# Performance work log

Hardware: AMD Instinct MI355X
Metric: run time of the kernel (lower is better)

## Reference

```python
import jax, jax.numpy as jnp
import numpy as np

B, S, H, NH = 8, 1024, 768, 12
DK = H // NH  # 64


def setup_inputs() -> dict:
    key = jax.random.key(0)
    ks = jax.random.split(key, 7)
    sc = 0.02
    return {
        "Q": jax.random.normal(ks[0], (B, S, H), jnp.float32),
        "K": jax.random.normal(ks[1], (B, S, H), jnp.float32),
        "V": jax.random.normal(ks[2], (B, S, H), jnp.float32),
        "Wq": jax.random.normal(ks[3], (H, H), jnp.float32) * sc,
        "Wk": jax.random.normal(ks[4], (H, H), jnp.float32) * sc,
        "Wv": jax.random.normal(ks[5], (H, H), jnp.float32) * sc,
        "Wo": jax.random.normal(ks[6], (H, H), jnp.float32) * sc,
    }


def reference(Q, K, V, Wq, Wk, Wv, Wo):
    # torch Linear(bias=False): y = x @ W.T, weight shape [out, in]
    q = jnp.einsum('bsh,oh->bso', Q, Wq).reshape(B, S, NH, DK)
    k = jnp.einsum('bsh,oh->bso', K, Wk).reshape(B, S, NH, DK)
    v = jnp.einsum('bsh,oh->bso', V, Wv).reshape(B, S, NH, DK)
    # naive SDPA per head: full [B,NH,S,S] score matrix, scale by sqrt(dk)
    scores = jnp.einsum('bqnd,bknd->bnqk', q, k) / jnp.sqrt(jnp.float32(DK))
    w = jax.nn.softmax(scores, axis=-1)
    c = jnp.einsum('bnqk,bknd->bqnd', w, v).reshape(B, S, H)
    return jnp.einsum('bsh,oh->bso', c, Wo)
```

## Files before the change

### kernel.cpp

```cpp
#include <hip/hip_runtime.h>
#include <hip/hip_bf16.h>

#define B_   8
#define S_   1024
#define H_   768
#define NH_  12
#define DK_  64
#define M_   (B_ * S_)

typedef __attribute__((ext_vector_type(8))) short          short8;
typedef __attribute__((ext_vector_type(8))) unsigned short ushort8;
typedef __attribute__((ext_vector_type(4))) unsigned short ushort4v;
typedef __attribute__((ext_vector_type(4))) float          f32x4;

__device__ __forceinline__ unsigned short f2bf(float x) {
    union { __hip_bfloat16 h; unsigned short u; } r;
    r.h = __float2bfloat16(x);
    return r.u;
}

__global__ __launch_bounds__(256)
void cvt_w(const float* __restrict__ w0, const float* __restrict__ w1,
           const float* __restrict__ w2, const float* __restrict__ w3,
           unsigned short* __restrict__ o0, unsigned short* __restrict__ o1,
           unsigned short* __restrict__ o2, unsigned short* __restrict__ o3)
{
    const int wsel = blockIdx.y;
    const float* src = (wsel == 0) ? w0 : (wsel == 1) ? w1 : (wsel == 2) ? w2 : w3;
    unsigned short* dst = (wsel == 0) ? o0 : (wsel == 1) ? o1 : (wsel == 2) ? o2 : o3;
    const float s = (wsel == 0) ? 0.125f * 1.44269504089f : 1.0f;
    const int i = blockIdx.x * 256 + threadIdx.x;
    const float4 x = ((const float4*)src)[i];
    ushort4v o;
    o[0] = f2bf(x.x * s); o[1] = f2bf(x.y * s);
    o[2] = f2bf(x.z * s); o[3] = f2bf(x.w * s);
    ((ushort4v*)dst)[i] = o;
}

template<bool A_BF16, bool OUT_BF16>
__global__ __launch_bounds__(256)
void gemm_bt(const void* __restrict__ A0, const void* __restrict__ A1,
             const void* __restrict__ A2,
             const unsigned short* __restrict__ W0,
             const unsigned short* __restrict__ W1,
             const unsigned short* __restrict__ W2,
             void* __restrict__ C0, void* __restrict__ C1, void* __restrict__ C2)
{
    __shared__ unsigned short As[128 * 32];
    __shared__ unsigned short Bs[128 * 32];

    const int tid  = threadIdx.x;
    const int z    = blockIdx.z;
    const int bm   = blockIdx.x, bn = blockIdx.y;
    const int w    = tid >> 6, lane = tid & 63;
    const int lg   = lane >> 4, lc = lane & 15;
    const int wm   = (w >> 1) * 64, wn = (w & 1) * 64;

    const void* Av = (z == 0) ? A0 : (z == 1) ? A1 : A2;
    const unsigned short* Bw = (z == 0) ? W0 : (z == 1) ? W1 : W2;
    void* Cv = (z == 0) ? C0 : (z == 1) ? C1 : C2;

    const float*          Af = (const float*)Av;
    const unsigned short* Ah = (const unsigned short*)Av;

    f32x4 acc[4][4] = {};

    for (int k0 = 0; k0 < H_; k0 += 32) {
        if (A_BF16) {
#pragma unroll
            for (int i = 0; i < 2; i++) {
                const int gI = i * 256 + tid;
                const int row = gI >> 2, c8 = (gI & 3) * 8;
                *(ushort8*)&As[row * 32 + c8] =
                    *(const ushort8*)&Ah[(size_t)(bm * 128 + row) * H_ + k0 + c8];
            }
        } else {
#pragma unroll
            for (int i = 0; i < 4; i++) {
                const int gI = i * 256 + tid;
                const int row = gI >> 3, c4 = (gI & 7) * 4;
                const float4 x = *(const float4*)&Af[(size_t)(bm * 128 + row) * H_ + k0 + c4];
                ushort4v o4;
                o4[0] = f2bf(x.x); o4[1] = f2bf(x.y);
                o4[2] = f2bf(x.z); o4[3] = f2bf(x.w);
                *(ushort4v*)&As[row * 32 + c4] = o4;
            }
        }
#pragma unroll
        for (int i = 0; i < 2; i++) {
            const int gI = i * 256 + tid;
            const int row = gI >> 2, c8 = (gI & 3) * 8;
            *(ushort8*)&Bs[row * 32 + c8] =
                *(const ushort8*)&Bw[(size_t)(bn * 128 + row) * H_ + k0 + c8];
        }
        __syncthreads();

        short8 af[4], bfr[4];
#pragma unroll
        for (int mi = 0; mi < 4; mi++)
            af[mi] = *(const short8*)&As[(wm + mi * 16 + lc) * 32 + lg * 8];
#pragma unroll
        for (int ni = 0; ni < 4; ni++)
            bfr[ni] = *(const short8*)&Bs[(wn + ni * 16 + lc) * 32 + lg * 8];
#pragma unroll
        for (int mi = 0; mi < 4; mi++)
#pragma unroll
            for (int ni = 0; ni < 4; ni++)
                acc[mi][ni] = __builtin_amdgcn_mfma_f32_16x16x32_bf16(
                    af[mi], bfr[ni], acc[mi][ni], 0, 0, 0);
        __syncthreads();
    }

#pragma unroll
    for (int mi = 0; mi < 4; mi++)
#pragma unroll
        for (int ni = 0; ni < 4; ni++)
#pragma unroll
            for (int reg = 0; reg < 4; reg++) {
                const int row = bm * 128 + wm + mi * 16 + lg * 4 + reg;
                const int col = bn * 128 + wn + ni * 16 + lc;
                if (OUT_BF16)
                    ((unsigned short*)Cv)[(size_t)row * H_ + col] = f2bf(acc[mi][ni][reg]);
                else
                    ((float*)Cv)[(size_t)row * H_ + col] = acc[mi][ni][reg];
            }
}

__global__ __launch_bounds__(256)
void attn(const unsigned short* __restrict__ q,
          const unsigned short* __restrict__ k,
          const unsigned short* __restrict__ v,
          unsigned short* __restrict__ c)
{
    __shared__ unsigned short Ks[64][72];
    __shared__ unsigned short Vt[64][72];
    __shared__ unsigned short Ps[128][72];

    const int tid  = threadIdx.x;
    const int qt   = blockIdx.x, h = blockIdx.y, b = blockIdx.z;
    const int wid  = tid >> 6;
    const int lane = tid & 63;
    const int lg   = lane >> 4, lc = lane & 15;
    const int r    = tid >> 2;
    const int d0   = (tid & 3) * 16;
    const int g    = tid & 3;
    const size_t base = (size_t)b * S_ * H_ + (size_t)h * DK_;

#pragma unroll
    for (int rr = 0; rr < 128; rr += 64) {
        const unsigned short* src = &q[base + (size_t)(qt * 128 + rr + r) * H_ + d0];
        *(ushort8*)&Ps[rr + r][d0]     = *(const ushort8*)src;
        *(ushort8*)&Ps[rr + r][d0 + 8] = *(const ushort8*)(src + 8);
    }
    __syncthreads();
    short8 aq[2][2];
#pragma unroll
    for (int m = 0; m < 2; m++)
#pragma unroll
        for (int ks = 0; ks < 2; ks++)
            aq[m][ks] = *(const short8*)&Ps[wid * 32 + m * 16 + lc][ks * 32 + lg * 8];

    f32x4 o[2][4] = {};
    float mrow[2][4], lrow[2][4];
#pragma unroll
    for (int m = 0; m < 2; m++)
#pragma unroll
        for (int i = 0; i < 4; i++) { mrow[m][i] = -1e30f; lrow[m][i] = 0.f; }

    for (int kt = 0; kt < S_ / 64; kt++) {
        {
            const unsigned short* ksrc = &k[base + (size_t)(kt * 64 + r) * H_ + d0];
            *(ushort8*)&Ks[r][d0]     = *(const ushort8*)ksrc;
            *(ushort8*)&Ks[r][d0 + 8] = *(const ushort8*)(ksrc + 8);
            const unsigned short* vsrc = &v[base + (size_t)(kt * 64 + r) * H_ + d0];
            const ushort8 v0 = *(const ushort8*)vsrc;
            const ushort8 v1 = *(const ushort8*)(vsrc + 8);
            const int colv = r ^ (g << 4);
#pragma unroll
            for (int j = 0; j < 8; j++) Vt[d0 + j][colv]     = v0[j];
#pragma unroll
            for (int j = 0; j < 8; j++) Vt[d0 + 8 + j][colv] = v1[j];
        }
        __syncthreads();

        f32x4 s[2][4] = {};
#pragma unroll
        for (int ni = 0; ni < 4; ni++) {
            const short8 bk0 = *(const short8*)&Ks[ni * 16 + lc][lg * 8];
            const short8 bk1 = *(const short8*)&Ks[ni * 16 + lc][32 + lg * 8];
            s[0][ni] = __builtin_amdgcn_mfma_f32_16x16x32_bf16(aq[0][0], bk0, s[0][ni], 0, 0, 0);
            s[0][ni] = __builtin_amdgcn_mfma_f32_16x16x32_bf16(aq[0][1], bk1, s[0][ni], 0, 0, 0);
            s[1][ni] = __builtin_amdgcn_mfma_f32_16x16x32_bf16(aq[1][0], bk0, s[1][ni], 0, 0, 0);
            s[1][ni] = __builtin_amdgcn_mfma_f32_16x16x32_bf16(aq[1][1], bk1, s[1][ni], 0, 0, 0);
        }

#pragma unroll
        for (int m = 0; m < 2; m++)
#pragma unroll
            for (int reg = 0; reg < 4; reg++) {
                float pm = fmaxf(fmaxf(s[m][0][reg], s[m][1][reg]),
                                 fmaxf(s[m][2][reg], s[m][3][reg]));
#pragma unroll
                for (int d = 1; d < 16; d <<= 1)
                    pm = fmaxf(pm, __shfl_xor(pm, d, 64));
                const float mnew  = fmaxf(mrow[m][reg], pm);
                const float scale = exp2f(mrow[m][reg] - mnew);
                float psum = 0.f;
#pragma unroll
                for (int ni = 0; ni < 4; ni++) {
                    const float p = exp2f(s[m][ni][reg] - mnew);
                    s[m][ni][reg] = p; psum += p;
                }
#pragma unroll
                for (int d = 1; d < 16; d <<= 1)
                    psum += __shfl_xor(psum, d, 64);
                lrow[m][reg] = lrow[m][reg] * scale + psum;
                mrow[m][reg] = mnew;
                o[m][0][reg] *= scale; o[m][1][reg] *= scale;
                o[m][2][reg] *= scale; o[m][3][reg] *= scale;
            }

#pragma unroll
        for (int m = 0; m < 2; m++)
#pragma unroll
            for (int ni = 0; ni < 4; ni++)
#pragma unroll
                for (int reg = 0; reg < 4; reg++)
                    Ps[wid * 32 + m * 16 + lg * 4 + reg][(ni * 16 + lc) ^ (lg << 4)] =
                        f2bf(s[m][ni][reg]);

        short8 pa[2][2];
#pragma unroll
        for (int m = 0; m < 2; m++)
#pragma unroll
            for (int ks = 0; ks < 2; ks++)
                pa[m][ks] = *(const short8*)
                    &Ps[wid * 32 + m * 16 + lc][(ks * 32 + lg * 8) ^ ((lc >> 2) << 4)];
#pragma unroll
        for (int ni = 0; ni < 4; ni++)
#pragma unroll
            for (int ks = 0; ks < 2; ks++) {
                const short8 bv = *(const short8*)
                    &Vt[ni * 16 + lc][(ks * 32 + lg * 8) ^ (ni << 4)];
                o[0][ni] = __builtin_amdgcn_mfma_f32_16x16x32_bf16(pa[0][ks], bv, o[0][ni], 0, 0, 0);
                o[1][ni] = __builtin_amdgcn_mfma_f32_16x16x32_bf16(pa[1][ks], bv, o[1][ni], 0, 0, 0);
            }
        __syncthreads();
    }

#pragma unroll
    for (int m = 0; m < 2; m++)
#pragma unroll
        for (int reg = 0; reg < 4; reg++) {
            const float inv = 1.0f / lrow[m][reg];
            const int row = qt * 128 + wid * 32 + m * 16 + lg * 4 + reg;
#pragma unroll
            for (int ni = 0; ni < 4; ni++)
                c[base + (size_t)row * H_ + ni * 16 + lc] = f2bf(o[m][ni][reg] * inv);
        }
}

extern "C" void kernel_launch(void* const* d_in, const int* in_sizes, int n_in,
                              void* d_out, int out_size, void* d_ws, size_t ws_size,
                              hipStream_t stream)
{
    const float* Q  = (const float*)d_in[0];
    const float* K  = (const float*)d_in[1];
    const float* V  = (const float*)d_in[2];
    const float* Wq = (const float*)d_in[3];
    const float* Wk = (const float*)d_in[4];
    const float* Wv = (const float*)d_in[5];
    const float* Wo = (const float*)d_in[6];

    unsigned short* qb = (unsigned short*)d_ws;
    unsigned short* kb = qb + (size_t)M_ * H_;
    unsigned short* vb = kb + (size_t)M_ * H_;
    unsigned short* cb = vb + (size_t)M_ * H_;
    unsigned short* wq = cb + (size_t)M_ * H_;
    unsigned short* wk = wq + (size_t)H_ * H_;
    unsigned short* wv = wk + (size_t)H_ * H_;
    unsigned short* wo = wv + (size_t)H_ * H_;

    cvt_w<<<dim3(H_ * H_ / 4 / 256, 4), 256, 0, stream>>>(
        Wq, Wk, Wv, Wo, wq, wk, wv, wo);

    gemm_bt<false, true><<<dim3(M_ / 128, H_ / 128, 3), 256, 0, stream>>>(
        Q, K, V, wq, wk, wv, qb, kb, vb);

    attn<<<dim3(S_ / 128, NH_, B_), 256, 0, stream>>>(qb, kb, vb, cb);

    gemm_bt<true, false><<<dim3(M_ / 128, H_ / 128, 1), 256, 0, stream>>>(
        cb, cb, cb, wo, wo, wo, d_out, d_out, d_out);
}
```

Baseline: 180.8 us.

## Compute transposed scores in attention and pass P via shuffles instead of LDS

The QK^T MFMA now has its operands swapped, so each lane holds the scores for a single query row. The row max and sum then need only two cross-lane shuffles instead of four per register. The probability tile is packed to bf16 with v_cvt_pk_bf16_f32 and rearranged into the PV A-operand layout with register shuffles, which removes the Ps shared buffer, its stores and loads, and a sync. Q fragments are read straight from global memory, and the per-row scale is broadcast by shuffle. This trades LDS traffic for more cross-lane shuffle and select instructions.

```diff
diff --git a/kernel.cpp b/kernel.cpp
--- a/kernel.cpp
+++ b/kernel.cpp
@@ -17,6 +17,12 @@
     union { __hip_bfloat16 h; unsigned short u; } r;
     r.h = __float2bfloat16(x);
     return r.u;
+}
+
+__device__ __forceinline__ unsigned cvtpk_bf16(float lo, float hi) {
+    unsigned r;
+    asm("v_cvt_pk_bf16_f32 %0, %1, %2" : "=v"(r) : "v"(lo), "v"(hi));
+    return r;
 }
 
 __global__ __launch_bounds__(256)
@@ -134,7 +140,6 @@
 {
     __shared__ unsigned short Ks[64][72];
     __shared__ unsigned short Vt[64][72];
-    __shared__ unsigned short Ps[128][72];
 
     const int tid  = threadIdx.x;
     const int qt   = blockIdx.x, h = blockIdx.y, b = blockIdx.z;
@@ -146,26 +151,16 @@
     const int g    = tid & 3;
     const size_t base = (size_t)b * S_ * H_ + (size_t)h * DK_;
 
-#pragma unroll
-    for (int rr = 0; rr < 128; rr += 64) {
-        const unsigned short* src = &q[base + (size_t)(qt * 128 + rr + r) * H_ + d0];
-        *(ushort8*)&Ps[rr + r][d0]     = *(const ushort8*)src;
-        *(ushort8*)&Ps[rr + r][d0 + 8] = *(const ushort8*)(src + 8);
-    }
-    __syncthreads();
     short8 aq[2][2];
 #pragma unroll
     for (int m = 0; m < 2; m++)
 #pragma unroll
         for (int ks = 0; ks < 2; ks++)
-            aq[m][ks] = *(const short8*)&Ps[wid * 32 + m * 16 + lc][ks * 32 + lg * 8];
+            aq[m][ks] = *(const short8*)
+                &q[base + (size_t)(qt * 128 + wid * 32 + m * 16 + lc) * H_ + ks * 32 + lg * 8];
 
     f32x4 o[2][4] = {};
-    float mrow[2][4], lrow[2][4];
-#pragma unroll
-    for (int m = 0; m < 2; m++)
-#pragma unroll
-        for (int i = 0; i < 4; i++) { mrow[m][i] = -1e30f; lrow[m][i] = 0.f; }
+    float mrow[2] = {-1e30f, -1e30f}, lrow[2] = {0.f, 0.f};
 
     for (int kt = 0; kt < S_ / 64; kt++) {
         {
@@ -183,59 +178,81 @@
         }
         __syncthreads();
 
-        f32x4 s[2][4] = {};
-#pragma unroll
-        for (int ni = 0; ni < 4; ni++) {
-            const short8 bk0 = *(const short8*)&Ks[ni * 16 + lc][lg * 8];
-            const short8 bk1 = *(const short8*)&Ks[ni * 16 + lc][32 + lg * 8];
-            s[0][ni] = __builtin_amdgcn_mfma_f32_16x16x32_bf16(aq[0][0], bk0, s[0][ni], 0, 0, 0);
-            s[0][ni] = __builtin_amdgcn_mfma_f32_16x16x32_bf16(aq[0][1], bk1, s[0][ni], 0, 0, 0);
-            s[1][ni] = __builtin_amdgcn_mfma_f32_16x16x32_bf16(aq[1][0], bk0, s[1][ni], 0, 0, 0);
-            s[1][ni] = __builtin_amdgcn_mfma_f32_16x16x32_bf16(aq[1][1], bk1, s[1][ni], 0, 0, 0);
-        }
-
+        f32x4 st[2][4] = {};
+#pragma unroll
+        for (int ni = 0; ni < 4; ni++)
+#pragma unroll
+            for (int ks = 0; ks < 2; ks++) {
+                const short8 bk = *(const short8*)&Ks[ni * 16 + lc][ks * 32 + lg * 8];
+                st[0][ni] = __builtin_amdgcn_mfma_f32_16x16x32_bf16(bk, aq[0][ks], st[0][ni], 0, 0, 0);
+                st[1][ni] = __builtin_amdgcn_mfma_f32_16x16x32_bf16(bk, aq[1][ks], st[1][ni], 0, 0, 0);
+            }
+
+        unsigned pw[2][4][2];
+#pragma unroll
+        for (int m = 0; m < 2; m++) {
+            float pm = st[m][0][0];
+#pragma unroll
+            for (int ni = 0; ni < 4; ni++)
+#pragma unroll
+                for (int reg = 0; reg < 4; reg++)
+                    pm = fmaxf(pm, st[m][ni][reg]);
+            pm = fmaxf(pm, __shfl_xor(pm, 16, 64));
+            pm = fmaxf(pm, __shfl_xor(pm, 32, 64));
+            const float mnew  = fmaxf(mrow[m], pm);
+            const float scale = exp2f(mrow[m] - mnew);
+            float psum = 0.f;
+#pragma unroll
+            for (int ni = 0; ni < 4; ni++)
+#pragma unroll
+                for (int reg = 0; reg < 4; reg++) {
+                    const float p = exp2f(st[m][ni][reg] - mnew);
+                    st[m][ni][reg] = p; psum += p;
+                }
+            psum += __shfl_xor(psum, 16, 64);
+            psum += __shfl_xor(psum, 32, 64);
+            lrow[m] = lrow[m] * scale + psum;
+            mrow[m] = mnew;
+
+            float scr[4];
+#pragma unroll
+            for (int reg = 0; reg < 4; reg++)
+                scr[reg] = __shfl(scale, lg * 4 + reg, 64);
+#pragma unroll
+            for (int ni = 0; ni < 4; ni++)
+#pragma unroll
+                for (int reg = 0; reg < 4; reg++)
+                    o[m][ni][reg] *= scr[reg];
+
+#pragma unroll
+            for (int ni = 0; ni < 4; ni++) {
+                pw[m][ni][0] = cvtpk_bf16(st[m][ni][0], st[m][ni][1]);
+                pw[m][ni][1] = cvtpk_bf16(st[m][ni][2], st[m][ni][3]);
+            }
+        }
+
+        const int sl0 = lc + ((lg & 1) << 5);
+        const int sl1 = sl0 + 16;
+        const bool hi = (lg >> 1) != 0;
+        short8 pa[2][2];
 #pragma unroll
         for (int m = 0; m < 2; m++)
 #pragma unroll
-            for (int reg = 0; reg < 4; reg++) {
-                float pm = fmaxf(fmaxf(s[m][0][reg], s[m][1][reg]),
-                                 fmaxf(s[m][2][reg], s[m][3][reg]));
-#pragma unroll
-                for (int d = 1; d < 16; d <<= 1)
-                    pm = fmaxf(pm, __shfl_xor(pm, d, 64));
-                const float mnew  = fmaxf(mrow[m][reg], pm);
-                const float scale = exp2f(mrow[m][reg] - mnew);
-                float psum = 0.f;
-#pragma unroll
-                for (int ni = 0; ni < 4; ni++) {
-                    const float p = exp2f(s[m][ni][reg] - mnew);
-                    s[m][ni][reg] = p; psum += p;
-                }
-#pragma unroll
-                for (int d = 1; d < 16; d <<= 1)
-                    psum += __shfl_xor(psum, d, 64);
-                lrow[m][reg] = lrow[m][reg] * scale + psum;
-                mrow[m][reg] = mnew;
-                o[m][0][reg] *= scale; o[m][1][reg] *= scale;
-                o[m][2][reg] *= scale; o[m][3][reg] *= scale;
-            }
-
-#pragma unroll
-        for (int m = 0; m < 2; m++)
-#pragma unroll
-            for (int ni = 0; ni < 4; ni++)
-#pragma unroll
-                for (int reg = 0; reg < 4; reg++)
-                    Ps[wid * 32 + m * 16 + lg * 4 + reg][(ni * 16 + lc) ^ (lg << 4)] =
-                        f2bf(s[m][ni][reg]);
-
-        short8 pa[2][2];
-#pragma unroll
-        for (int m = 0; m < 2; m++)
-#pragma unroll
-            for (int ks = 0; ks < 2; ks++)
-                pa[m][ks] = *(const short8*)
-                    &Ps[wid * 32 + m * 16 + lc][(ks * 32 + lg * 8) ^ ((lc >> 2) << 4)];
+            for (int ks = 0; ks < 2; ks++) {
+                const unsigned lo0 = pw[m][2 * ks][0],     lo1 = pw[m][2 * ks][1];
+                const unsigned hi0 = pw[m][2 * ks + 1][0], hi1 = pw[m][2 * ks + 1][1];
+                union { unsigned u[4]; short8 s8; } pk;
+                const unsigned a0l = __shfl(lo0, sl0, 64), a0h = __shfl(hi0, sl0, 64);
+                const unsigned a1l = __shfl(lo1, sl0, 64), a1h = __shfl(hi1, sl0, 64);
+                const unsigned a2l = __shfl(lo0, sl1, 64), a2h = __shfl(hi0, sl1, 64);
+                const unsigned a3l = __shfl(lo1, sl1, 64), a3h = __shfl(hi1, sl1, 64);
+                pk.u[0] = hi ? a0h : a0l;
+                pk.u[1] = hi ? a1h : a1l;
+                pk.u[2] = hi ? a2h : a2l;
+                pk.u[3] = hi ? a3h : a3l;
+                pa[m][ks] = pk.s8;
+            }
+
 #pragma unroll
         for (int ni = 0; ni < 4; ni++)
 #pragma unroll
@@ -249,15 +266,17 @@
     }
 
 #pragma unroll
-    for (int m = 0; m < 2; m++)
+    for (int m = 0; m < 2; m++) {
+        const float iv = 1.0f / lrow[m];
 #pragma unroll
         for (int reg = 0; reg < 4; reg++) {
-            const float inv = 1.0f / lrow[m][reg];
+            const float ivr = __shfl(iv, lg * 4 + reg, 64);
             const int row = qt * 128 + wid * 32 + m * 16 + lg * 4 + reg;
 #pragma unroll
             for (int ni = 0; ni < 4; ni++)
-                c[base + (size_t)row * H_ + ni * 16 + lc] = f2bf(o[m][ni][reg] * inv);
-        }
+                c[base + (size_t)row * H_ + ni * 16 + lc] = f2bf(o[m][ni][reg] * ivr);
+        }
+    }
 }
 
 extern "C" void kernel_launch(void* const* d_in, const int* in_sizes, int n_in,
```

Measured after the change: 155.3 us. 1.16x faster.
